# Kernel tuning notes

Hardware: AMD Instinct MI355X
Metric: run time of the kernel (lower is better)

The kernel has to match this reference:

```python
import jax, jax.numpy as jnp
import numpy as np
import math

B, S, D, H, DQ, DV, P = 8, 1024, 512, 8, 64, 64, 32


def _layer_norm(x, g, b, eps=1e-5):
    mu = jnp.mean(x, axis=-1, keepdims=True)
    var = jnp.mean((x - mu) ** 2, axis=-1, keepdims=True)
    return (x - mu) * jax.lax.rsqrt(var + eps) * g + b


def setup_inputs() -> dict:
    key = jax.random.key(0)
    ks = jax.random.split(key, 12)
    s = 0.02
    x = jax.random.normal(ks[0], (B, S, D), dtype=jnp.float32)
    lengths = jax.random.randint(ks[1], (B,), S // 2, S + 1)  # avoid fully-masked rows
    return {
        "x": x,
        "ln_g": jnp.ones((D,), jnp.float32),
        "ln_b": jnp.zeros((D,), jnp.float32),
        "Wk": jax.random.normal(ks[2], (D, H * DQ), jnp.float32) * s,
        "bk": jnp.zeros((H * DQ,), jnp.float32),
        "Wv": jax.random.normal(ks[3], (D, H * DV), jnp.float32) * s,
        "bv": jnp.zeros((H * DV,), jnp.float32),
        "pos": jax.random.normal(ks[4], (1, S, S, P), jnp.float32) * s,  # learned pos table
        "wp": jax.random.normal(ks[5], (P,), jnp.float32) * s,  # map_pos Linear(P,1) weight
        "bp": jnp.zeros((), jnp.float32),  # map_pos bias
        "Wo": jax.random.normal(ks[6], (H * DV, D), jnp.float32) * s,
        "bo": jnp.zeros((D,), jnp.float32),
        "key_value_sequence_lengths": lengths,
    }


def reference(x, ln_g, ln_b, Wk, bk, Wv, bv, pos, wp, bp, Wo, bo, key_value_sequence_lengths):
    # self-attention, encoder (no causal mask), 'kv+pos' branch, eval mode (dropout off)
    xn = _layer_norm(x, ln_g, ln_b)
    k = (xn @ Wk + bk).reshape(B, S, H, DQ).transpose(0, 2, 1, 3)  # [B,H,S,DQ]
    v = (xn @ Wv + bv).reshape(B, S, H, DV).transpose(0, 2, 1, 3)  # [B,H,S,DV]

    # kv+pos: scores use keys twice (tmp = keys since N == M)
    scores = jnp.einsum("bhnd,bhmd->bhnm", k, k) / math.sqrt(H)
    # map_pos(scores[...,None] + pos) == scores * sum(wp) + pos@wp + bp (linear, fused)
    bias = jnp.einsum("qkp,p->qk", pos[0], wp) + bp  # [S,S]
    attn = scores * jnp.sum(wp) + bias[None, None]
    attn = attn / math.sqrt(DQ)

    key_ok = jnp.arange(S)[None, None, None, :] < key_value_sequence_lengths[:, None, None, None]
    attn = jnp.where(key_ok, attn, -jnp.inf)
    probs = jax.nn.softmax(attn, axis=-1)  # [B,H,S,S]

    out = jnp.einsum("bhnm,bhmd->bhnd", probs, v)
    out = out.transpose(0, 2, 1, 3).reshape(B, S, H * DV)
    seq = out @ Wo + bo + x
    return seq, probs
```

## Files before the change

### kernel.cpp

```cpp
#include <hip/hip_runtime.h>
#include <hip/hip_bf16.h>


typedef __attribute__((ext_vector_type(8))) short short8;
typedef __attribute__((ext_vector_type(4))) short short4v;
typedef __attribute__((ext_vector_type(4))) float float4v;

#define MFMA16(a, b, c) __builtin_amdgcn_mfma_f32_16x16x32_bf16((a), (b), (c), 0, 0, 0)

__device__ inline unsigned short f2bf(float f) {
    unsigned u = __builtin_bit_cast(unsigned, f);
    unsigned r = (u + 0x7FFFu + ((u >> 16) & 1u)) >> 16;
    return (unsigned short)r;
}
__device__ inline float bf2f(unsigned short h) {
    unsigned u = ((unsigned)h) << 16;
    return __builtin_bit_cast(float, u);
}

__device__ __forceinline__ void async16(const void* g, void* l) {
    __builtin_amdgcn_global_load_lds(
        (const __attribute__((address_space(1))) unsigned int*)(unsigned long long)g,
        (__attribute__((address_space(3))) unsigned int*)(unsigned)(unsigned long long)l,
        16, 0, 0);
}

__global__ __launch_bounds__(256) void ln_kernel(const float* __restrict__ x,
                                                 const float* __restrict__ g,
                                                 const float* __restrict__ b,
                                                 unsigned short* __restrict__ xn) {
    int wave = threadIdx.x >> 6;
    int lane = threadIdx.x & 63;
    size_t row = (size_t)blockIdx.x * 4 + wave;
    const float4* x4 = (const float4*)(x + row * 512);
    float4 v0 = x4[lane];
    float4 v1 = x4[lane + 64];
    float s = v0.x + v0.y + v0.z + v0.w + v1.x + v1.y + v1.z + v1.w;
    for (int o = 32; o; o >>= 1) s += __shfl_xor(s, o);
    float mu = s * (1.0f / 512.0f);
    float d0x = v0.x - mu, d0y = v0.y - mu, d0z = v0.z - mu, d0w = v0.w - mu;
    float d1x = v1.x - mu, d1y = v1.y - mu, d1z = v1.z - mu, d1w = v1.w - mu;
    float q = d0x * d0x + d0y * d0y + d0z * d0z + d0w * d0w +
              d1x * d1x + d1y * d1y + d1z * d1z + d1w * d1w;
    for (int o = 32; o; o >>= 1) q += __shfl_xor(q, o);
    float rs = rsqrtf(q * (1.0f / 512.0f) + 1e-5f);
    const float4* g4 = (const float4*)g;
    const float4* b4 = (const float4*)b;
    float4 g0 = g4[lane], g1 = g4[lane + 64];
    float4 b0 = b4[lane], b1 = b4[lane + 64];
    short4v o0, o1;
    o0[0] = (short)f2bf(d0x * rs * g0.x + b0.x);
    o0[1] = (short)f2bf(d0y * rs * g0.y + b0.y);
    o0[2] = (short)f2bf(d0z * rs * g0.z + b0.z);
    o0[3] = (short)f2bf(d0w * rs * g0.w + b0.w);
    o1[0] = (short)f2bf(d1x * rs * g1.x + b1.x);
    o1[1] = (short)f2bf(d1y * rs * g1.y + b1.y);
    o1[2] = (short)f2bf(d1z * rs * g1.z + b1.z);
    o1[3] = (short)f2bf(d1w * rs * g1.w + b1.w);
    *(short4v*)(xn + row * 512 + lane * 4) = o0;
    *(short4v*)(xn + row * 512 + 256 + lane * 4) = o1;
}

__global__ __launch_bounds__(256) void wconv_kernel(const float* __restrict__ Wk,
                                                    const float* __restrict__ Wv,
                                                    const float* __restrict__ Wo,
                                                    unsigned short* __restrict__ WkT,
                                                    unsigned short* __restrict__ WvT,
                                                    unsigned short* __restrict__ WoT) {
    int i = blockIdx.x * 256 + threadIdx.x;
    const float* src = (blockIdx.y == 0) ? Wk : (blockIdx.y == 1) ? Wv : Wo;
    unsigned short* dst = (blockIdx.y == 0) ? WkT : (blockIdx.y == 1) ? WvT : WoT;
    int k = i >> 9, n = i & 511;
    dst[n * 512 + k] = f2bf(src[i]);
}

__global__ __launch_bounds__(256) void bias_kernel(const float* __restrict__ pos,
                                                   const float* __restrict__ wp,
                                                   const float* __restrict__ bp,
                                                   float* __restrict__ biasS) {
    size_t idx = (size_t)blockIdx.x * 256 + threadIdx.x;
    const float4* p4 = (const float4*)pos + idx * 8;
    const float4* w4 = (const float4*)wp;
    float acc = 0.f;
#pragma unroll
    for (int j = 0; j < 8; j++) {
        float4 p = p4[j];
        float4 w = w4[j];
        acc += p.x * w.x + p.y * w.y + p.z * w.z + p.w * w.w;
    }
    biasS[idx] = (acc + bp[0]) * 0.125f;
}

__global__ __launch_bounds__(256) void proj_kernel(const unsigned short* __restrict__ xn,
                                                   const unsigned short* __restrict__ WkT,
                                                   const unsigned short* __restrict__ WvT,
                                                   const float* __restrict__ bk,
                                                   const float* __restrict__ bv,
                                                   unsigned short* __restrict__ K,
                                                   unsigned short* __restrict__ Vt) {
    __shared__ unsigned short sa[128 * 32];
    __shared__ unsigned short sb[128 * 32];
    int z = blockIdx.z;
    const unsigned short* Bm = z ? WvT : WkT;
    const float* bias = z ? bv : bk;
    int m0 = blockIdx.y * 128, n0 = blockIdx.x * 128;
    int lane = threadIdx.x & 63, w = threadIdx.x >> 6;
    int l15 = lane & 15, quad = lane >> 4, q8 = quad * 8;
    int wm = w >> 1, wn = w & 1;
    int srow = w * 16 + (lane >> 2);
    int scol = (lane & 3) * 8;
    float4v acc[4][4] = {};
    for (int k0 = 0; k0 < 512; k0 += 32) {
        __syncthreads();
        async16(xn + (size_t)(m0 + srow) * 512 + k0 + scol, &sa[w * 512]);
        async16(xn + (size_t)(m0 + 64 + srow) * 512 + k0 + scol, &sa[2048 + w * 512]);
        async16(Bm + (size_t)(n0 + srow) * 512 + k0 + scol, &sb[w * 512]);
        async16(Bm + (size_t)(n0 + 64 + srow) * 512 + k0 + scol, &sb[2048 + w * 512]);
        __syncthreads();
        short8 af[4], bf[4];
#pragma unroll
        for (int t = 0; t < 4; t++)
            af[t] = *(const short8*)&sa[(wm * 64 + t * 16 + l15) * 32 + q8];
#pragma unroll
        for (int t = 0; t < 4; t++)
            bf[t] = *(const short8*)&sb[(wn * 64 + t * 16 + l15) * 32 + q8];
#pragma unroll
        for (int mt = 0; mt < 4; mt++)
#pragma unroll
            for (int nt = 0; nt < 4; nt++)
                acc[mt][nt] = MFMA16(af[mt], bf[nt], acc[mt][nt]);
    }
#pragma unroll
    for (int mt = 0; mt < 4; mt++)
#pragma unroll
        for (int nt = 0; nt < 4; nt++)
#pragma unroll
            for (int r = 0; r < 4; r++) {
                int m = m0 + wm * 64 + mt * 16 + quad * 4 + r;
                int n = n0 + wn * 64 + nt * 16 + l15;
                float v = acc[mt][nt][r] + bias[n];
                int b = m >> 10, s = m & 1023;
                int h = n >> 6, d = n & 63;
                if (z == 0)
                    K[(((size_t)b * 8 + h) * 1024 + s) * 64 + d] = f2bf(v);
                else
                    Vt[(((size_t)b * 8 + h) * 64 + d) * 1024 + s] = f2bf(v);
            }
}

__global__ __launch_bounds__(256) void attn_kernel(const unsigned short* __restrict__ K,
                                                   const unsigned short* __restrict__ Vt,
                                                   const float* __restrict__ biasS,
                                                   const float* __restrict__ wp,
                                                   const int* __restrict__ lens,
                                                   float* __restrict__ probs,
                                                   unsigned short* __restrict__ outb) {
    __shared__ unsigned short sc[16 * 1032];
    int bid = blockIdx.x;
    int bh = bid >> 6, qt = bid & 63;
    int b = bh >> 3, h = bh & 7;
    int q0 = qt * 16;
    int lane = threadIdx.x & 63;
    int w = threadIdx.x >> 6;
    int l15 = lane & 15, quad = lane >> 4;
    int q8 = quad * 8;
    int len = lens[b];

    float swp = 0.f;
#pragma unroll
    for (int j = 0; j < 32; j++) swp += wp[j];
    float c1 = swp * 0.04419417382415922f;

    const unsigned short* Kbh = K + (size_t)bh * 1024 * 64;
    short8 a00 = *(const short8*)(Kbh + (size_t)(q0 + l15) * 64 + q8);
    short8 a01 = *(const short8*)(Kbh + (size_t)(q0 + l15) * 64 + q8 + 32);

    for (int i = 0; i < 16; i++) {
        int n0 = (i * 4 + w) * 16;
        short8 b0 = *(const short8*)(Kbh + (size_t)(n0 + l15) * 64 + q8);
        short8 b1 = *(const short8*)(Kbh + (size_t)(n0 + l15) * 64 + q8 + 32);
        float4v acc0 = {};
        acc0 = MFMA16(a00, b0, acc0);
        acc0 = MFMA16(a01, b1, acc0);
        int key = n0 + l15;
        bool ok = key < len;
#pragma unroll
        for (int r = 0; r < 4; r++) {
            int row0 = quad * 4 + r;
            float lg0 = ok ? acc0[r] * c1 + biasS[(size_t)(q0 + row0) * 1024 + key] : -1e30f;
            sc[row0 * 1032 + key] = f2bf(lg0);
        }
    }
    __syncthreads();

    for (int rr = 0; rr < 4; rr++) {
        int row = w * 4 + rr;
        float v[16];
        float mx = -1e30f;
#pragma unroll
        for (int j = 0; j < 16; j++) {
            v[j] = bf2f(sc[row * 1032 + lane + j * 64]);
            mx = fmaxf(mx, v[j]);
        }
        for (int o = 32; o; o >>= 1) mx = fmaxf(mx, __shfl_xor(mx, o));
        float s = 0.f;
#pragma unroll
        for (int j = 0; j < 16; j++) {
            v[j] = __expf(v[j] - mx);
            s += v[j];
        }
        for (int o = 32; o; o >>= 1) s += __shfl_xor(s, o);
        float inv = 1.0f / s;
        float* prow = probs + ((size_t)bh * 1024 + q0 + row) * 1024;
#pragma unroll
        for (int j = 0; j < 16; j++) {
            float p = v[j] * inv;
            sc[row * 1032 + lane + j * 64] = f2bf(p);
            __builtin_nontemporal_store(p, prow + lane + j * 64);
        }
    }
    __syncthreads();

    int nv = w * 16;
    const unsigned short* Vbh = Vt + (size_t)bh * 64 * 1024;
    float4v o0 = {};
    for (int ks = 0; ks < 32; ks++) {
        int k0 = ks * 32;
        short8 bb = *(const short8*)(Vbh + (size_t)(nv + l15) * 1024 + k0 + q8);
        short8 p0 = *(const short8*)&sc[l15 * 1032 + k0 + q8];
        o0 = MFMA16(p0, bb, o0);
    }
#pragma unroll
    for (int r = 0; r < 4; r++) {
        int row = quad * 4 + r;
        int qa = q0 + row;
        outb[((size_t)b * 1024 + qa) * 512 + h * 64 + nv + l15] = f2bf(o0[r]);
    }
}

__global__ __launch_bounds__(256) void oproj_kernel(const unsigned short* __restrict__ outb,
                                                    const unsigned short* __restrict__ WoT,
                                                    const float* __restrict__ bo,
                                                    const float* __restrict__ x,
                                                    float* __restrict__ seq) {
    __shared__ unsigned short sa[128 * 32];
    __shared__ unsigned short sb[128 * 32];
    int m0 = blockIdx.y * 128, n0 = blockIdx.x * 128;
    int lane = threadIdx.x & 63, w = threadIdx.x >> 6;
    int l15 = lane & 15, quad = lane >> 4, q8 = quad * 8;
    int wm = w >> 1, wn = w & 1;
    int srow = w * 16 + (lane >> 2);
    int scol = (lane & 3) * 8;
    float4v acc[4][4] = {};
    for (int k0 = 0; k0 < 512; k0 += 32) {
        __syncthreads();
        async16(outb + (size_t)(m0 + srow) * 512 + k0 + scol, &sa[w * 512]);
        async16(outb + (size_t)(m0 + 64 + srow) * 512 + k0 + scol, &sa[2048 + w * 512]);
        async16(WoT + (size_t)(n0 + srow) * 512 + k0 + scol, &sb[w * 512]);
        async16(WoT + (size_t)(n0 + 64 + srow) * 512 + k0 + scol, &sb[2048 + w * 512]);
        __syncthreads();
        short8 af[4], bf[4];
#pragma unroll
        for (int t = 0; t < 4; t++)
            af[t] = *(const short8*)&sa[(wm * 64 + t * 16 + l15) * 32 + q8];
#pragma unroll
        for (int t = 0; t < 4; t++)
            bf[t] = *(const short8*)&sb[(wn * 64 + t * 16 + l15) * 32 + q8];
#pragma unroll
        for (int mt = 0; mt < 4; mt++)
#pragma unroll
            for (int nt = 0; nt < 4; nt++)
                acc[mt][nt] = MFMA16(af[mt], bf[nt], acc[mt][nt]);
    }
#pragma unroll
    for (int mt = 0; mt < 4; mt++)
#pragma unroll
        for (int nt = 0; nt < 4; nt++)
#pragma unroll
            for (int r = 0; r < 4; r++) {
                int m = m0 + wm * 64 + mt * 16 + quad * 4 + r;
                int n = n0 + wn * 64 + nt * 16 + l15;
                seq[(size_t)m * 512 + n] = acc[mt][nt][r] + bo[n] + x[(size_t)m * 512 + n];
            }
}

extern "C" void kernel_launch(void* const* d_in, const int* in_sizes, int n_in,
                              void* d_out, int out_size, void* d_ws, size_t ws_size,
                              hipStream_t stream) {
    const float* x    = (const float*)d_in[0];
    const float* ln_g = (const float*)d_in[1];
    const float* ln_b = (const float*)d_in[2];
    const float* Wk   = (const float*)d_in[3];
    const float* bk   = (const float*)d_in[4];
    const float* Wv   = (const float*)d_in[5];
    const float* bv   = (const float*)d_in[6];
    const float* pos  = (const float*)d_in[7];
    const float* wp   = (const float*)d_in[8];
    const float* bp   = (const float*)d_in[9];
    const float* Wo   = (const float*)d_in[10];
    const float* bo   = (const float*)d_in[11];
    const int* lens   = (const int*)d_in[12];

    unsigned short* WkT  = (unsigned short*)d_ws;
    unsigned short* WvT  = WkT + 512 * 512;
    unsigned short* WoT  = WvT + 512 * 512;
    unsigned short* xn   = WoT + 512 * 512;
    unsigned short* Kb   = xn + (size_t)8192 * 512;
    unsigned short* Vt   = Kb + (size_t)64 * 1024 * 64;
    unsigned short* outb = Vt + (size_t)64 * 64 * 1024;
    float* biasS = (float*)(outb + (size_t)8192 * 512);

    float* seq = (float*)d_out;
    float* probs = seq + (size_t)8192 * 512;

    hipLaunchKernelGGL(wconv_kernel, dim3(1024, 3), dim3(256), 0, stream,
                       Wk, Wv, Wo, WkT, WvT, WoT);
    hipLaunchKernelGGL(ln_kernel, dim3(2048), dim3(256), 0, stream, x, ln_g, ln_b, xn);
    hipLaunchKernelGGL(bias_kernel, dim3(4096), dim3(256), 0, stream, pos, wp, bp, biasS);
    hipLaunchKernelGGL(proj_kernel, dim3(4, 64, 2), dim3(256), 0, stream,
                       xn, WkT, WvT, bk, bv, Kb, Vt);
    hipLaunchKernelGGL(attn_kernel, dim3(4096), dim3(256), 0, stream,
                       Kb, Vt, biasS, wp, lens, probs, outb);
    hipLaunchKernelGGL(oproj_kernel, dim3(4, 64), dim3(256), 0, stream,
                       outb, WoT, bo, x, seq);
}
```

Before: 559.2 us.

## Store positional bias transposed in bf16 and regroup attention blocks for locality

The bias kernel now reduces pos with a coalesced wave-level shuffle and writes a transposed bf16 table, so the attention kernel can load four query rows per key as one short4 instead of doing strided fp32 gathers. Attention block indices are remapped so neighbouring blocks share query tiles and hit the same bias lines in cache. Barriers that wait only on LDS counters replace __syncthreads, the QK loop is unrolled, and the PV loop uses two accumulators for more MFMA overlap. The cost is bias precision dropping to bf16 and a scattered 2-byte transposed write in the bias kernel.

Result: no change. 563.9 us (+0.8%).

```diff
diff --git a/kernel.cpp b/kernel.cpp
--- a/kernel.cpp
+++ b/kernel.cpp
@@ -23,6 +23,13 @@
         (const __attribute__((address_space(1))) unsigned int*)(unsigned long long)g,
         (__attribute__((address_space(3))) unsigned int*)(unsigned)(unsigned long long)l,
         16, 0, 0);
+}
+
+__device__ __forceinline__ void barrier_lds() {
+    asm volatile("s_waitcnt lgkmcnt(0)" ::: "memory");
+    __builtin_amdgcn_sched_barrier(0);
+    __builtin_amdgcn_s_barrier();
+    __builtin_amdgcn_sched_barrier(0);
 }
 
 __global__ __launch_bounds__(256) void ln_kernel(const float* __restrict__ x,
@@ -77,18 +84,27 @@
 __global__ __launch_bounds__(256) void bias_kernel(const float* __restrict__ pos,
                                                    const float* __restrict__ wp,
                                                    const float* __restrict__ bp,
-                                                   float* __restrict__ biasS) {
-    size_t idx = (size_t)blockIdx.x * 256 + threadIdx.x;
-    const float4* p4 = (const float4*)pos + idx * 8;
-    const float4* w4 = (const float4*)wp;
-    float acc = 0.f;
-#pragma unroll
-    for (int j = 0; j < 8; j++) {
-        float4 p = p4[j];
-        float4 w = w4[j];
-        acc += p.x * w.x + p.y * w.y + p.z * w.z + p.w * w.w;
-    }
-    biasS[idx] = (acc + bp[0]) * 0.125f;
+                                                   unsigned short* __restrict__ biasT) {
+    int lane = threadIdx.x & 63;
+    int w = threadIdx.x >> 6;
+    size_t wbase = ((size_t)blockIdx.x * 4 + w) * 64;
+    float4 wv = ((const float4*)wp)[lane & 7];
+    float bias0 = bp[0];
+#pragma unroll
+    for (int t = 0; t < 8; t++) {
+        size_t p0 = wbase + (size_t)t * 8;
+        const float4* src = (const float4*)(pos + p0 * 32);
+        float4 d = src[lane];
+        float s = d.x * wv.x + d.y * wv.y + d.z * wv.z + d.w * wv.w;
+        s += __shfl_xor(s, 1);
+        s += __shfl_xor(s, 2);
+        s += __shfl_xor(s, 4);
+        if ((lane & 7) == 0) {
+            size_t p = p0 + (lane >> 3);
+            int q = (int)(p >> 10), k = (int)(p & 1023);
+            biasT[(size_t)k * 1024 + q] = f2bf((s + bias0) * 0.125f);
+        }
+    }
 }
 
 __global__ __launch_bounds__(256) void proj_kernel(const unsigned short* __restrict__ xn,
@@ -150,14 +166,16 @@
 
 __global__ __launch_bounds__(256) void attn_kernel(const unsigned short* __restrict__ K,
                                                    const unsigned short* __restrict__ Vt,
-                                                   const float* __restrict__ biasS,
+                                                   const unsigned short* __restrict__ biasT,
                                                    const float* __restrict__ wp,
                                                    const int* __restrict__ lens,
                                                    float* __restrict__ probs,
                                                    unsigned short* __restrict__ outb) {
     __shared__ unsigned short sc[16 * 1032];
     int bid = blockIdx.x;
-    int bh = bid >> 6, qt = bid & 63;
+    int sup = bid >> 6, wi = bid & 63;
+    int bh = (sup & ~7) | (wi >> 3);
+    int qt = ((sup & 7) << 3) | (wi & 7);
     int b = bh >> 3, h = bh & 7;
     int q0 = qt * 16;
     int lane = threadIdx.x & 63;
@@ -175,6 +193,7 @@
     short8 a00 = *(const short8*)(Kbh + (size_t)(q0 + l15) * 64 + q8);
     short8 a01 = *(const short8*)(Kbh + (size_t)(q0 + l15) * 64 + q8 + 32);
 
+#pragma unroll 2
     for (int i = 0; i < 16; i++) {
         int n0 = (i * 4 + w) * 16;
         short8 b0 = *(const short8*)(Kbh + (size_t)(n0 + l15) * 64 + q8);
@@ -184,14 +203,15 @@
         acc0 = MFMA16(a01, b1, acc0);
         int key = n0 + l15;
         bool ok = key < len;
+        short4v bb4 = *(const short4v*)(biasT + (size_t)key * 1024 + q0 + quad * 4);
 #pragma unroll
         for (int r = 0; r < 4; r++) {
             int row0 = quad * 4 + r;
-            float lg0 = ok ? acc0[r] * c1 + biasS[(size_t)(q0 + row0) * 1024 + key] : -1e30f;
+            float lg0 = ok ? acc0[r] * c1 + bf2f((unsigned short)bb4[r]) : -1e30f;
             sc[row0 * 1032 + key] = f2bf(lg0);
         }
     }
-    __syncthreads();
+    barrier_lds();
 
     for (int rr = 0; rr < 4; rr++) {
         int row = w * 4 + rr;
@@ -219,17 +239,21 @@
             __builtin_nontemporal_store(p, prow + lane + j * 64);
         }
     }
-    __syncthreads();
+    barrier_lds();
 
     int nv = w * 16;
     const unsigned short* Vbh = Vt + (size_t)bh * 64 * 1024;
-    float4v o0 = {};
-    for (int ks = 0; ks < 32; ks++) {
+    float4v o0a = {}, o0b = {};
+    for (int ks = 0; ks < 32; ks += 2) {
         int k0 = ks * 32;
-        short8 bb = *(const short8*)(Vbh + (size_t)(nv + l15) * 1024 + k0 + q8);
+        short8 bb0 = *(const short8*)(Vbh + (size_t)(nv + l15) * 1024 + k0 + q8);
         short8 p0 = *(const short8*)&sc[l15 * 1032 + k0 + q8];
-        o0 = MFMA16(p0, bb, o0);
-    }
+        short8 bb1 = *(const short8*)(Vbh + (size_t)(nv + l15) * 1024 + k0 + 32 + q8);
+        short8 p1 = *(const short8*)&sc[l15 * 1032 + k0 + 32 + q8];
+        o0a = MFMA16(p0, bb0, o0a);
+        o0b = MFMA16(p1, bb1, o0b);
+    }
+    float4v o0 = o0a + o0b;
 #pragma unroll
     for (int r = 0; r < 4; r++) {
         int row = quad * 4 + r;
@@ -308,7 +332,7 @@
     unsigned short* Kb   = xn + (size_t)8192 * 512;
     unsigned short* Vt   = Kb + (size_t)64 * 1024 * 64;
     unsigned short* outb = Vt + (size_t)64 * 64 * 1024;
-    float* biasS = (float*)(outb + (size_t)8192 * 512);
+    unsigned short* biasT = outb + (size_t)8192 * 512;
 
     float* seq = (float*)d_out;
     float* probs = seq + (size_t)8192 * 512;
@@ -316,11 +340,11 @@
     hipLaunchKernelGGL(wconv_kernel, dim3(1024, 3), dim3(256), 0, stream,
                        Wk, Wv, Wo, WkT, WvT, WoT);
     hipLaunchKernelGGL(ln_kernel, dim3(2048), dim3(256), 0, stream, x, ln_g, ln_b, xn);
-    hipLaunchKernelGGL(bias_kernel, dim3(4096), dim3(256), 0, stream, pos, wp, bp, biasS);
+    hipLaunchKernelGGL(bias_kernel, dim3(4096), dim3(256), 0, stream, pos, wp, bp, biasT);
     hipLaunchKernelGGL(proj_kernel, dim3(4, 64, 2), dim3(256), 0, stream,
                        xn, WkT, WvT, bk, bv, Kb, Vt);
     hipLaunchKernelGGL(attn_kernel, dim3(4096), dim3(256), 0, stream,
-                       Kb, Vt, biasS, wp, lens, probs, outb);
+                       Kb, Vt, biasT, wp, lens, probs, outb);
     hipLaunchKernelGGL(oproj_kernel, dim3(4, 64), dim3(256), 0, stream,
                        outb, WoT, bo, x, seq);
 }
```
